# Kernel tuning notes

Hardware: AMD Instinct MI355X
Metric: run time of the kernel (lower is better)

The kernel has to match this reference:

```python
import jax, jax.numpy as jnp
import numpy as np
from jax import lax

B, C_E, C_D, H, W, K = 64, 768, 512, 28, 28, 3
EPS = 1e-6


def setup_inputs() -> dict:
    key = jax.random.key(0)
    k1, k2, k3, k4, k5 = jax.random.split(key, 5)
    bcff = jax.random.normal(k1, (B, C_E, H, W), dtype=jnp.float32)
    cur_active = jax.random.bernoulli(k2, p=0.25, shape=(B, 1, H, W))
    # learned mask token, trunc-normal(std=0.02)
    mask_token = jnp.clip(0.02 * jax.random.normal(k3, (1, C_E, 1, 1), dtype=jnp.float32), -0.02, 0.02)
    ln_weight = jnp.ones((C_E,), dtype=jnp.float32)
    ln_bias = jnp.zeros((C_E,), dtype=jnp.float32)
    fan_in = C_E * K * K
    bound = 1.0 / np.sqrt(fan_in)
    conv_w = jax.random.uniform(k4, (C_D, C_E, K, K), minval=-bound, maxval=bound, dtype=jnp.float32)
    conv_b = jax.random.uniform(k5, (C_D,), minval=-bound, maxval=bound, dtype=jnp.float32)
    return {"bcff": bcff, "cur_active": cur_active, "mask_token": mask_token,
            "ln_weight": ln_weight, "ln_bias": ln_bias, "conv_w": conv_w, "conv_b": conv_b}


def reference(bcff, cur_active, mask_token, ln_weight, ln_bias, conv_w, conv_b):
    # Sparse channels-first LayerNorm: per-position LN over C. Original gathers
    # active positions, LNs them, scatters back into zeros. Since inactive
    # positions are subsequently replaced by mask tokens via torch.where, the
    # dense-LN-then-where form below is mathematically identical.
    mu = jnp.mean(bcff, axis=1, keepdims=True)                      # [B,1,H,W]
    var = jnp.mean((bcff - mu) ** 2, axis=1, keepdims=True)         # biased var, like torch LN
    normed = (bcff - mu) * lax.rsqrt(var + EPS)
    normed = ln_weight[None, :, None, None] * normed + ln_bias[None, :, None, None]
    # masked token fill: active positions keep normed features, inactive get mask token
    x = jnp.where(cur_active, normed, mask_token)                   # [B,C_E,H,W]
    # densify_proj: 3x3 conv, stride 1, padding 1, with bias
    y = lax.conv_general_dilated(x, conv_w, window_strides=(1, 1), padding="SAME",
                                 dimension_numbers=("NCHW", "OIHW", "NCHW"))
    return y + conv_b[None, :, None, None]
```

## Files before the change

kernel.cpp:

```cpp
#include <hip/hip_runtime.h>
#include <cstdint>
#include <cstddef>

#define CE 768
#define CD 512
#define NB 64
#define HH 28
#define WW 28
#define HP 30
#define WP 30
#define POS 784
#define M_TOT 50176
#define K_TOT 6912

typedef _Float16 f16x8 __attribute__((ext_vector_type(8)));
typedef _Float16 f16x4 __attribute__((ext_vector_type(4)));
typedef float f32x4 __attribute__((ext_vector_type(4)));

__global__ void prep_w_kernel(const float* __restrict__ cw, _Float16* __restrict__ wT) {
  int co = blockIdx.x;
  const float* src = cw + (size_t)co * CE * 9;
  _Float16* dst = wT + (size_t)co * K_TOT;
  for (int j = threadIdx.x; j < K_TOT; j += blockDim.x) {
    int tap = j / CE;
    int ci = j - tap * CE;
    dst[j] = (_Float16)src[ci * 9 + tap];
  }
}

__global__ void __launch_bounds__(512) ln_fused_kernel(
    const float* __restrict__ bcff, const int* __restrict__ act,
    const float* __restrict__ mtok, const float* __restrict__ gamma,
    const float* __restrict__ beta, _Float16* __restrict__ xp) {
  int b = blockIdx.x / HP, ph = blockIdx.x % HP;
  _Float16* xrow = xp + ((size_t)(b * HP + ph)) * WP * CE;
  const int tid = threadIdx.x;
  if (ph == 0 || ph == HP - 1) {
    uint4* p = (uint4*)xrow;
    uint4 z = make_uint4(0, 0, 0, 0);
    for (int j = tid; j < (WP * CE * 2) / 16; j += 512) p[j] = z;
    return;
  }
  int h = ph - 1;
  {
    uint4 z = make_uint4(0, 0, 0, 0);
    uint4* p0 = (uint4*)xrow;
    uint4* p1 = (uint4*)(xrow + (size_t)(WP - 1) * CE);
    for (int j = tid; j < (CE * 2) / 16; j += 512) { p0[j] = z; p1[j] = z; }
  }

  __shared__ float tile[CE * 29];
  __shared__ float s_mean[WW], s_rstd[WW];
  __shared__ int s_act[WW];

  const float* src = bcff + ((size_t)b * CE * HH + h) * WW;
#pragma unroll 6
  for (int i = tid; i < CE * WW; i += 512) {
    int cc = i / WW, w = i - cc * WW;
    tile[cc * 29 + w] = src[(size_t)cc * (HH * WW) + w];
  }
  if (tid < WW) s_act[tid] = act[b * POS + h * WW + tid];
  __syncthreads();

  if (tid < WW * 16) {
    int w = tid >> 4, j = tid & 15;
    float s = 0.f, ss = 0.f;
#pragma unroll 8
    for (int c = j; c < CE; c += 16) {
      float v = tile[c * 29 + w];
      s += v; ss += v * v;
    }
#pragma unroll
    for (int d = 8; d; d >>= 1) {
      s += __shfl_down(s, d, 16);
      ss += __shfl_down(ss, d, 16);
    }
    if (j == 0) {
      float mu = s * (1.f / 768.f);
      float var = ss * (1.f / 768.f) - mu * mu;
      s_mean[w] = mu;
      s_rstd[w] = rsqrtf(var + 1e-6f);
    }
  }
  __syncthreads();

  for (int i = tid; i < WW * 192; i += 512) {
    int w = i / 192, q = i - w * 192;
    int c = q * 4;
    f16x4 o;
    if (s_act[w]) {
      float mu = s_mean[w], rs = s_rstd[w];
#pragma unroll
      for (int j = 0; j < 4; ++j)
        o[j] = (_Float16)((tile[(c + j) * 29 + w] - mu) * rs * gamma[c + j] + beta[c + j]);
    } else {
#pragma unroll
      for (int j = 0; j < 4; ++j) o[j] = (_Float16)mtok[c + j];
    }
    *(f16x4*)(xrow + (size_t)(w + 1) * CE + c) = o;
  }
}

__global__ void conv_gemm_kernel(const _Float16* __restrict__ xp, const _Float16* __restrict__ wT,
                                 const float* __restrict__ bias, float* __restrict__ out) {
  __shared__ _Float16 smem[8192];
  char* sAb = (char*)smem;
  char* sBb = sAb + 8192;

  const int t = threadIdx.x;
  const int lane = t & 63, wv = t >> 6;
  const int m0 = blockIdx.x * 128;
  const int n0 = blockIdx.y * 128;

  const int r0 = t >> 2;
  const int ks = (((t & 3) ^ ((t >> 3) & 3))) * 8;
  const int m_a0 = m0 + r0;
  const int m_a1 = m0 + r0 + 64;
  int b0 = m_a0 / POS, p0 = m_a0 - b0 * POS;
  int b1 = m_a1 / POS, p1 = m_a1 - b1 * POS;
  int h0 = p0 / WW, w0 = p0 - h0 * WW;
  int h1 = p1 / WW, w1 = p1 - h1 * WW;
  const _Float16* gA0 = xp + ((size_t)((b0 * HP + h0) * WP + w0)) * CE + ks;
  const _Float16* gA1 = xp + ((size_t)((b1 * HP + h1) * WP + w1)) * CE + ks;
  const _Float16* gB0 = wT + (size_t)(n0 + r0) * K_TOT + ks;
  const _Float16* gB1 = wT + (size_t)(n0 + r0 + 64) * K_TOT + ks;

  char* ldsA0 = sAb + wv * 1024;
  char* ldsA1 = sAb + 4096 + wv * 1024;
  char* ldsB0 = sBb + wv * 1024;
  char* ldsB1 = sBb + 4096 + wv * 1024;

  const int wm = wv & 1, wn = wv >> 1;
  const int swz = ((lane >> 4) ^ (((lane & 15) >> 1) & 3)) * 16;
  const int afrag_off = (wm * 64 + (lane & 15)) * 64 + swz;
  const int bfrag_off = (wn * 64 + (lane & 15)) * 64 + swz;

  f32x4 acc[4][4] = {};

  int aoff = 0, kin = 0, dw = 0;
  for (int kk = 0; kk < K_TOT / 32; ++kk) {
    __builtin_amdgcn_global_load_lds((__attribute__((address_space(1))) void*)(gA0 + aoff),
                                     (__attribute__((address_space(3))) void*)ldsA0, 16, 0, 0);
    __builtin_amdgcn_global_load_lds((__attribute__((address_space(1))) void*)(gA1 + aoff),
                                     (__attribute__((address_space(3))) void*)ldsA1, 16, 0, 0);
    __builtin_amdgcn_global_load_lds((__attribute__((address_space(1))) void*)(gB0 + kk * 32),
                                     (__attribute__((address_space(3))) void*)ldsB0, 16, 0, 0);
    __builtin_amdgcn_global_load_lds((__attribute__((address_space(1))) void*)(gB1 + kk * 32),
                                     (__attribute__((address_space(3))) void*)ldsB1, 16, 0, 0);
    __syncthreads();

    f16x8 af[4], bf[4];
#pragma unroll
    for (int i = 0; i < 4; ++i) af[i] = *(const f16x8*)(sAb + afrag_off + i * 1024);
#pragma unroll
    for (int i = 0; i < 4; ++i) bf[i] = *(const f16x8*)(sBb + bfrag_off + i * 1024);
#pragma unroll
    for (int mi = 0; mi < 4; ++mi)
#pragma unroll
      for (int ni = 0; ni < 4; ++ni)
        acc[mi][ni] = __builtin_amdgcn_mfma_f32_16x16x32_f16(af[mi], bf[ni], acc[mi][ni], 0, 0, 0);
    __syncthreads();

    kin += 32; aoff += 32;
    if (kin == 768) { kin = 0; ++dw; if (dw == 3) { dw = 0; aoff += 27 * 768; } }
  }

  float bv[4];
#pragma unroll
  for (int ni = 0; ni < 4; ++ni) bv[ni] = bias[n0 + wn * 64 + ni * 16 + (lane & 15)];
#pragma unroll
  for (int mi = 0; mi < 4; ++mi) {
    int mbase = m0 + wm * 64 + mi * 16 + (lane >> 4) * 4;
    int b = mbase / POS, pos = mbase - b * POS;
    float* obase = out + (size_t)b * CD * POS + pos;
#pragma unroll
    for (int ni = 0; ni < 4; ++ni) {
      int co = n0 + wn * 64 + ni * 16 + (lane & 15);
      f32x4 v = acc[mi][ni];
      v += bv[ni];
      *(f32x4*)(obase + (size_t)co * POS) = v;
    }
  }
}

extern "C" void kernel_launch(void* const* d_in, const int* in_sizes, int n_in,
                              void* d_out, int out_size, void* d_ws, size_t ws_size,
                              hipStream_t stream) {
  const float* bcff = (const float*)d_in[0];
  const int* cur_active = (const int*)d_in[1];
  const float* mask_token = (const float*)d_in[2];
  const float* ln_w = (const float*)d_in[3];
  const float* ln_b = (const float*)d_in[4];
  const float* conv_w = (const float*)d_in[5];
  const float* conv_b = (const float*)d_in[6];
  float* out = (float*)d_out;

  char* ws = (char*)d_ws;
  _Float16* xp = (_Float16*)ws;
  _Float16* wT = (_Float16*)(ws + 88473600);

  prep_w_kernel<<<dim3(CD), dim3(256), 0, stream>>>(conv_w, wT);
  ln_fused_kernel<<<dim3(NB * HP), dim3(512), 0, stream>>>(bcff, cur_active, mask_token,
                                                           ln_w, ln_b, xp);
  conv_gemm_kernel<<<dim3(M_TOT / 128, CD / 128), dim3(256), 0, stream>>>(xp, wT, conv_b, out);
}
```

Baseline: 777.5 us.

## Restructure conv as padded-pixel strip GEMM reusing A tile across nine taps

```diff
diff --git a/kernel.cpp b/kernel.cpp
--- a/kernel.cpp
+++ b/kernel.cpp
@@ -12,6 +12,8 @@
 #define POS 784
 #define M_TOT 50176
 #define K_TOT 6912
+#define MP 57600
+#define XP_PIX 57728
 
 typedef _Float16 f16x8 __attribute__((ext_vector_type(8)));
 typedef _Float16 f16x4 __attribute__((ext_vector_type(4)));
@@ -49,7 +51,7 @@
     for (int j = tid; j < (CE * 2) / 16; j += 512) { p0[j] = z; p1[j] = z; }
   }
 
-  __shared__ float tile[CE * 29];
+  __shared__ _Float16 tile[CE * 29];
   __shared__ float s_mean[WW], s_rstd[WW];
   __shared__ int s_act[WW];
 
@@ -57,7 +59,7 @@
 #pragma unroll 6
   for (int i = tid; i < CE * WW; i += 512) {
     int cc = i / WW, w = i - cc * WW;
-    tile[cc * 29 + w] = src[(size_t)cc * (HH * WW) + w];
+    tile[cc * 29 + w] = (_Float16)src[(size_t)cc * (HH * WW) + w];
   }
   if (tid < WW) s_act[tid] = act[b * POS + h * WW + tid];
   __syncthreads();
@@ -67,7 +69,7 @@
     float s = 0.f, ss = 0.f;
 #pragma unroll 8
     for (int c = j; c < CE; c += 16) {
-      float v = tile[c * 29 + w];
+      float v = (float)tile[c * 29 + w];
       s += v; ss += v * v;
     }
 #pragma unroll
@@ -92,7 +94,7 @@
       float mu = s_mean[w], rs = s_rstd[w];
 #pragma unroll
       for (int j = 0; j < 4; ++j)
-        o[j] = (_Float16)((tile[(c + j) * 29 + w] - mu) * rs * gamma[c + j] + beta[c + j]);
+        o[j] = (_Float16)(((float)tile[(c + j) * 29 + w] - mu) * rs * gamma[c + j] + beta[c + j]);
     } else {
 #pragma unroll
       for (int j = 0; j < 4; ++j) o[j] = (_Float16)mtok[c + j];
@@ -101,84 +103,103 @@
   }
 }
 
-__global__ void conv_gemm_kernel(const _Float16* __restrict__ xp, const _Float16* __restrict__ wT,
-                                 const float* __restrict__ bias, float* __restrict__ out) {
-  __shared__ _Float16 smem[8192];
+#define GLDS(src, dst) __builtin_amdgcn_global_load_lds( \
+    (const __attribute__((address_space(1))) void*)(src), \
+    (__attribute__((address_space(3))) void*)(dst), 16, 0, 0)
+
+__global__ void __launch_bounds__(512) conv_strip_kernel(
+    const _Float16* __restrict__ xp, const _Float16* __restrict__ wT,
+    const float* __restrict__ bias, float* __restrict__ out) {
+  __shared__ _Float16 smem[24576];
   char* sAb = (char*)smem;
-  char* sBb = sAb + 8192;
+  char* sBb = sAb + 12288;
 
   const int t = threadIdx.x;
   const int lane = t & 63, wv = t >> 6;
-  const int m0 = blockIdx.x * 128;
-  const int n0 = blockIdx.y * 128;
-
-  const int r0 = t >> 2;
-  const int ks = (((t & 3) ^ ((t >> 3) & 3))) * 8;
-  const int m_a0 = m0 + r0;
-  const int m_a1 = m0 + r0 + 64;
-  int b0 = m_a0 / POS, p0 = m_a0 - b0 * POS;
-  int b1 = m_a1 / POS, p1 = m_a1 - b1 * POS;
-  int h0 = p0 / WW, w0 = p0 - h0 * WW;
-  int h1 = p1 / WW, w1 = p1 - h1 * WW;
-  const _Float16* gA0 = xp + ((size_t)((b0 * HP + h0) * WP + w0)) * CE + ks;
-  const _Float16* gA1 = xp + ((size_t)((b1 * HP + h1) * WP + w1)) * CE + ks;
-  const _Float16* gB0 = wT + (size_t)(n0 + r0) * K_TOT + ks;
-  const _Float16* gB1 = wT + (size_t)(n0 + r0 + 64) * K_TOT + ks;
-
-  char* ldsA0 = sAb + wv * 1024;
-  char* ldsA1 = sAb + 4096 + wv * 1024;
-  char* ldsB0 = sBb + wv * 1024;
-  char* ldsB1 = sBb + 4096 + wv * 1024;
-
-  const int wm = wv & 1, wn = wv >> 1;
-  const int swz = ((lane >> 4) ^ (((lane & 15) >> 1) & 3)) * 16;
-  const int afrag_off = (wm * 64 + (lane & 15)) * 64 + swz;
-  const int bfrag_off = (wn * 64 + (lane & 15)) * 64 + swz;
-
-  f32x4 acc[4][4] = {};
-
-  int aoff = 0, kin = 0, dw = 0;
-  for (int kk = 0; kk < K_TOT / 32; ++kk) {
-    __builtin_amdgcn_global_load_lds((__attribute__((address_space(1))) void*)(gA0 + aoff),
-                                     (__attribute__((address_space(3))) void*)ldsA0, 16, 0, 0);
-    __builtin_amdgcn_global_load_lds((__attribute__((address_space(1))) void*)(gA1 + aoff),
-                                     (__attribute__((address_space(3))) void*)ldsA1, 16, 0, 0);
-    __builtin_amdgcn_global_load_lds((__attribute__((address_space(1))) void*)(gB0 + kk * 32),
-                                     (__attribute__((address_space(3))) void*)ldsB0, 16, 0, 0);
-    __builtin_amdgcn_global_load_lds((__attribute__((address_space(1))) void*)(gB1 + kk * 32),
-                                     (__attribute__((address_space(3))) void*)ldsB1, 16, 0, 0);
+  const int nb = blockIdx.x & 7;
+  const int mb = blockIdx.x >> 3;
+  const int p0 = mb * 128;
+  const int n0 = nb * 64;
+
+  const int jj = (t & 3) ^ ((t >> 3) & 3);
+  const int pixA = t >> 2;
+  const _Float16* pA0 = xp + (size_t)(p0 + pixA) * CE + jj * 8;
+  const _Float16* pA1 = pA0 + (size_t)128 * CE;
+  const int rowB = (t >> 2) & 63;
+  const int hiB = t >> 8;
+  const _Float16* pB = wT + (size_t)(n0 + rowB) * K_TOT + jj * 8;
+  char* dA0 = sAb + wv * 1024;
+  char* dA1 = sAb + 8192 + wv * 1024;
+  char* dB0 = sBb + wv * 1024;
+
+  const int wm = wv >> 1, wn = wv & 1;
+  const int rowbase0 = wm * 32 + (lane & 15);
+  const int lq = lane >> 4;
+  const int bfrag_off = (wn * 32 + (lane & 15)) * 64 +
+                        ((lq ^ (((lane & 15) >> 1) & 3)) * 16);
+
+  f32x4 acc[2][2] = {};
+  const int tap_off[9] = {0, 1, 2, 30, 31, 32, 60, 61, 62};
+
+  for (int c24 = 0; c24 < 24; ++c24) {
+    const int koff = c24 * 32;
+    GLDS(pA0 + koff, dA0);
+    if (wv < 4) GLDS(pA1 + koff, dA1);
+#pragma unroll
+    for (int k = 0; k < 4; ++k)
+      GLDS(pB + (2 * k + hiB) * CE + koff, dB0 + 8192 * k);
+    if (wv < 4) GLDS(pB + 8 * CE + koff, dB0 + 32768);
     __syncthreads();
 
-    f16x8 af[4], bf[4];
-#pragma unroll
-    for (int i = 0; i < 4; ++i) af[i] = *(const f16x8*)(sAb + afrag_off + i * 1024);
-#pragma unroll
-    for (int i = 0; i < 4; ++i) bf[i] = *(const f16x8*)(sBb + bfrag_off + i * 1024);
-#pragma unroll
-    for (int mi = 0; mi < 4; ++mi)
-#pragma unroll
-      for (int ni = 0; ni < 4; ++ni)
-        acc[mi][ni] = __builtin_amdgcn_mfma_f32_16x16x32_f16(af[mi], bf[ni], acc[mi][ni], 0, 0, 0);
+#pragma unroll
+    for (int tap = 0; tap < 9; ++tap) {
+      const int rA = rowbase0 + tap_off[tap];
+      const char* aptr = sAb + rA * 64 + ((lq ^ ((rA >> 1) & 3)) * 16);
+      f16x8 a0 = *(const f16x8*)(aptr);
+      f16x8 a1 = *(const f16x8*)(aptr + 1024);
+      const char* bptr = sBb + tap * 4096 + bfrag_off;
+      f16x8 b0 = *(const f16x8*)(bptr);
+      f16x8 b1 = *(const f16x8*)(bptr + 1024);
+      acc[0][0] = __builtin_amdgcn_mfma_f32_16x16x32_f16(a0, b0, acc[0][0], 0, 0, 0);
+      acc[0][1] = __builtin_amdgcn_mfma_f32_16x16x32_f16(a0, b1, acc[0][1], 0, 0, 0);
+      acc[1][0] = __builtin_amdgcn_mfma_f32_16x16x32_f16(a1, b0, acc[1][0], 0, 0, 0);
+      acc[1][1] = __builtin_amdgcn_mfma_f32_16x16x32_f16(a1, b1, acc[1][1], 0, 0, 0);
+    }
     __syncthreads();
-
-    kin += 32; aoff += 32;
-    if (kin == 768) { kin = 0; ++dw; if (dw == 3) { dw = 0; aoff += 27 * 768; } }
-  }
-
-  float bv[4];
-#pragma unroll
-  for (int ni = 0; ni < 4; ++ni) bv[ni] = bias[n0 + wn * 64 + ni * 16 + (lane & 15)];
-#pragma unroll
-  for (int mi = 0; mi < 4; ++mi) {
-    int mbase = m0 + wm * 64 + mi * 16 + (lane >> 4) * 4;
-    int b = mbase / POS, pos = mbase - b * POS;
-    float* obase = out + (size_t)b * CD * POS + pos;
-#pragma unroll
-    for (int ni = 0; ni < 4; ++ni) {
-      int co = n0 + wn * 64 + ni * 16 + (lane & 15);
+  }
+
+  float bv[2];
+#pragma unroll
+  for (int ni = 0; ni < 2; ++ni) bv[ni] = bias[n0 + wn * 32 + ni * 16 + (lane & 15)];
+#pragma unroll
+  for (int mi = 0; mi < 2; ++mi) {
+    int g = p0 + wm * 32 + mi * 16 + (lane >> 4) * 4;
+    int b = g / 900;
+    int q = g - b * 900;
+    int ph = q / 30, pw = q - ph * 30;
+#pragma unroll
+    for (int ni = 0; ni < 2; ++ni) {
+      int co = n0 + wn * 32 + ni * 16 + (lane & 15);
       f32x4 v = acc[mi][ni];
       v += bv[ni];
-      *(f32x4*)(obase + (size_t)co * POS) = v;
+      float* obase = out + ((size_t)b * CD + co) * POS;
+      if (b < NB && ph < 28) {
+        if (pw <= 24) {
+          *(f32x4*)(obase + ph * 28 + pw) = v;
+        } else if (pw == 26) {
+          obase[ph * 28 + 26] = v[0];
+          obase[ph * 28 + 27] = v[1];
+        }
+      }
+      if (pw == 28) {
+        int b2 = b, ph2 = ph + 1;
+        if (ph2 == 30) { b2++; ph2 = 0; }
+        if (b2 < NB && ph2 < 28) {
+          float* o2 = out + ((size_t)b2 * CD + co) * POS + ph2 * 28;
+          o2[0] = v[2];
+          o2[1] = v[3];
+        }
+      }
     }
   }
 }
@@ -197,10 +218,10 @@
 
   char* ws = (char*)d_ws;
   _Float16* xp = (_Float16*)ws;
-  _Float16* wT = (_Float16*)(ws + 88473600);
+  _Float16* wT = (_Float16*)(ws + (size_t)XP_PIX * CE * 2);
 
   prep_w_kernel<<<dim3(CD), dim3(256), 0, stream>>>(conv_w, wT);
   ln_fused_kernel<<<dim3(NB * HP), dim3(512), 0, stream>>>(bcff, cur_active, mask_token,
                                                            ln_w, ln_b, xp);
-  conv_gemm_kernel<<<dim3(M_TOT / 128, CD / 128), dim3(256), 0, stream>>>(xp, wT, conv_b, out);
-}
+  conv_strip_kernel<<<dim3(450 * 8), dim3(512), 0, stream>>>(xp, wT, conv_b, out);
+}
```

After: 669.0 us. 14.0% less time.
